# Performance work log

Hardware: AMD Instinct MI355X
Metric: run time of the kernel (lower is better)

## Reference

```python
import jax, jax.numpy as jnp
import numpy as np

IN_FEATURES = 512
NUM_KNOTS = 64
XMIN = -3.0
XMAX = 3.0


def setup_inputs() -> dict:
    key = jax.random.key(0)
    kx, kc = jax.random.split(key)
    x = jax.random.normal(kx, (65536, IN_FEATURES), dtype=jnp.float32)
    coeffs = jax.random.normal(kc, (IN_FEATURES, NUM_KNOTS), dtype=jnp.float32) * 0.01
    return {"x": x, "coeffs": coeffs}


def reference(x, coeffs):
    # x: (B, F); coeffs: (F, K). Piecewise-linear spline per feature, summed over features.
    K = coeffs.shape[1]
    t = (x - XMIN) / (XMAX - XMIN) * (K - 1)          # (B, F)
    t0 = jnp.clip(jnp.floor(t).astype(jnp.int32), 0, K - 2)
    w1 = t - t0.astype(t.dtype)
    w0 = 1.0 - w1
    feat_idx = jnp.arange(coeffs.shape[0])[None, :]    # (1, F) broadcast with (B, F) indices
    c0 = coeffs[feat_idx, t0]                          # (B, F) gather
    c1 = coeffs[feat_idx, t0 + 1]
    return jnp.sum(w0 * c0 + w1 * c1, axis=1)          # (B,)
```

## Files before the change

kernel.cpp:

```cpp
#include <hip/hip_runtime.h>


#define TILE_B 64
#define CHUNK_F 128
#define NCHUNK 4
#define LSTRIDE 129
#define FPW 32

__global__ __launch_bounds__(256, 4)
void spline_kernel(const float* __restrict__ x,
                   const float* __restrict__ coeffs,
                   float* __restrict__ out)
{
    __shared__ float ldsX[TILE_B * LSTRIDE];
    __shared__ float ldsR[4 * TILE_B];

    const int t    = threadIdx.x;
    const int lane = t & 63;
    const int w    = t >> 6;
    const long rowBase = (long)blockIdx.x * TILE_B;

    float acc0 = 0.0f, acc1 = 0.0f;

    for (int ch = 0; ch < NCHUNK; ++ch) {
        const int cbase = ch * CHUNK_F;
        __syncthreads();
        #pragma unroll
        for (int s = 0; s < 8; ++s) {
            int i4 = s * 256 + t;
            int r  = i4 >> 5;
            int c4 = i4 & 31;
            const float4 v = *reinterpret_cast<const float4*>(
                x + (rowBase + r) * 512 + cbase + c4 * 4);
            float* dst = &ldsX[r * LSTRIDE + c4 * 4];
            dst[0] = v.x; dst[1] = v.y; dst[2] = v.z; dst[3] = v.w;
        }
        __syncthreads();
        #pragma unroll 8
        for (int j = 0; j < FPW; ++j) {
            const int fc = w * FPW + j;
            const int f  = cbase + fc;
            const float cr = coeffs[f * 64 + lane];
            const float xv = ldsX[lane * LSTRIDE + fc];
            const float tt  = (xv + 3.0f) * 10.5f;
            float t0f = floorf(tt);
            t0f = fminf(fmaxf(t0f, 0.0f), 62.0f);
            const int t0 = (int)t0f;
            const float c0 = __shfl(cr, t0, 64);
            const float c1 = __shfl(cr, t0 + 1, 64);
            const float w1 = tt - t0f;
            if (j & 1) acc1 += c0 + w1 * (c1 - c0);
            else       acc0 += c0 + w1 * (c1 - c0);
        }
    }

    ldsR[w * TILE_B + lane] = acc0 + acc1;
    __syncthreads();
    if (t < TILE_B) {
        float r = ldsR[t] + ldsR[TILE_B + t] + ldsR[2 * TILE_B + t] + ldsR[3 * TILE_B + t];
        out[rowBase + t] = r;
    }
}

extern "C" void kernel_launch(void* const* d_in, const int* in_sizes, int n_in,
                              void* d_out, int out_size, void* d_ws, size_t ws_size,
                              hipStream_t stream) {
    const float* x      = (const float*)d_in[0];
    const float* coeffs = (const float*)d_in[1];
    float* out = (float*)d_out;
    (void)in_sizes; (void)n_in; (void)out_size; (void)d_ws; (void)ws_size;

    dim3 grid(65536 / TILE_B);
    dim3 block(256);
    spline_kernel<<<grid, block, 0, stream>>>(x, coeffs, out);
}
```

Baseline: 34.82 us.

## Rewrite spline kernel with packed bf16 coefficient table in LDS and lane-per-feature layout

Each block now builds a 64KB LDS table per 256-feature half. Every entry packs a bf16 base coefficient and a bf16 slope, and entries are rotated per feature to avoid bank conflicts. Each lane reads x with float4 loads straight from global memory, does one LDS lookup per feature instead of two shuffles, and reduces rows with butterfly shuffles. Blocks are 1024 threads covering 128 rows. This removes the x staging through LDS and the cross-lane shuffles, but rounding coefficients to bf16 loses precision and may break tolerance. Each block also rebuilds the coefficient table.

```diff
diff --git a/kernel.cpp b/kernel.cpp
--- a/kernel.cpp
+++ b/kernel.cpp
@@ -1,65 +1,75 @@
 #include <hip/hip_runtime.h>
+#include <stdint.h>
 
 
-#define TILE_B 64
-#define CHUNK_F 128
-#define NCHUNK 4
-#define LSTRIDE 129
-#define FPW 32
+#define ROWS_PER_BLOCK 128
 
-__global__ __launch_bounds__(256, 4)
+__device__ __forceinline__ uint32_t bf16_rne(float v) {
+    uint32_t u = __float_as_uint(v);
+    return (u + 0x7fffu + ((u >> 16) & 1u)) >> 16;
+}
+
+__global__ __launch_bounds__(1024, 4)
 void spline_kernel(const float* __restrict__ x,
                    const float* __restrict__ coeffs,
                    float* __restrict__ out)
 {
-    __shared__ float ldsX[TILE_B * LSTRIDE];
-    __shared__ float ldsR[4 * TILE_B];
+    __shared__ uint32_t T[256 * 64];
 
-    const int t    = threadIdx.x;
-    const int lane = t & 63;
-    const int w    = t >> 6;
-    const long rowBase = (long)blockIdx.x * TILE_B;
+    const int tid  = threadIdx.x;
+    const int lane = tid & 63;
+    const int w    = tid >> 6;
+    const long rowBase = (long)blockIdx.x * ROWS_PER_BLOCK;
+    const float lf   = (float)lane;
+    const float tadd = 31.5f + lf;
+    const float hi   = lf + 62.0f;
 
-    float acc0 = 0.0f, acc1 = 0.0f;
+    float accR[8] = {0.f, 0.f, 0.f, 0.f, 0.f, 0.f, 0.f, 0.f};
 
-    for (int ch = 0; ch < NCHUNK; ++ch) {
-        const int cbase = ch * CHUNK_F;
+    #pragma unroll
+    for (int c = 0; c < 2; ++c) {
         __syncthreads();
         #pragma unroll
-        for (int s = 0; s < 8; ++s) {
-            int i4 = s * 256 + t;
-            int r  = i4 >> 5;
-            int c4 = i4 & 31;
-            const float4 v = *reinterpret_cast<const float4*>(
-                x + (rowBase + r) * 512 + cbase + c4 * 4);
-            float* dst = &ldsX[r * LSTRIDE + c4 * 4];
-            dst[0] = v.x; dst[1] = v.y; dst[2] = v.z; dst[3] = v.w;
+        for (int it = 0; it < 16; ++it) {
+            const int idx = it * 1024 + tid;
+            const int fl  = idx >> 6;
+            const int k   = idx & 63;
+            const int gi  = c * 16384 + idx;
+            const float c0 = coeffs[gi];
+            const float c1 = coeffs[gi + (k < 63 ? 1 : 0)];
+            const int kp  = (k + (fl >> 2)) & 63;
+            T[(idx & ~63) | kp] = (bf16_rne(c0) << 16) | bf16_rne(c1 - c0);
         }
         __syncthreads();
-        #pragma unroll 8
-        for (int j = 0; j < FPW; ++j) {
-            const int fc = w * FPW + j;
-            const int f  = cbase + fc;
-            const float cr = coeffs[f * 64 + lane];
-            const float xv = ldsX[lane * LSTRIDE + fc];
-            const float tt  = (xv + 3.0f) * 10.5f;
-            float t0f = floorf(tt);
-            t0f = fminf(fmaxf(t0f, 0.0f), 62.0f);
-            const int t0 = (int)t0f;
-            const float c0 = __shfl(cr, t0, 64);
-            const float c1 = __shfl(cr, t0 + 1, 64);
-            const float w1 = tt - t0f;
-            if (j & 1) acc1 += c0 + w1 * (c1 - c0);
-            else       acc0 += c0 + w1 * (c1 - c0);
+
+        const float* xb = x + (rowBase + w * 8) * 512 + c * 256 + lane * 4;
+        #pragma unroll 2
+        for (int r = 0; r < 8; ++r) {
+            const float4 v = *reinterpret_cast<const float4*>(xb + r * 512);
+            float a = 0.f;
+            #pragma unroll
+            for (int q = 0; q < 4; ++q) {
+                const float xv  = (q == 0) ? v.x : (q == 1) ? v.y : (q == 2) ? v.z : v.w;
+                const float tt  = xv * 10.5f + tadd;
+                const float t0f = fminf(fmaxf(floorf(tt), lf), hi);
+                const uint32_t g = T[(lane << 8) + (q << 6) + (((int)t0f) & 63)];
+                a += __uint_as_float(g & 0xffff0000u)
+                   + (tt - t0f) * __uint_as_float(g << 16);
+            }
+            accR[r] += a;
         }
     }
 
-    ldsR[w * TILE_B + lane] = acc0 + acc1;
-    __syncthreads();
-    if (t < TILE_B) {
-        float r = ldsR[t] + ldsR[TILE_B + t] + ldsR[2 * TILE_B + t] + ldsR[3 * TILE_B + t];
-        out[rowBase + t] = r;
+    float stash = 0.f;
+    #pragma unroll
+    for (int r = 0; r < 8; ++r) {
+        float s = accR[r];
+        #pragma unroll
+        for (int m = 1; m < 64; m <<= 1)
+            s += __shfl_xor(s, m, 64);
+        if (lane == r) stash = s;
     }
+    if (lane < 8) out[rowBase + w * 8 + lane] = stash;
 }
 
 extern "C" void kernel_launch(void* const* d_in, const int* in_sizes, int n_in,
@@ -70,7 +80,7 @@
     float* out = (float*)d_out;
     (void)in_sizes; (void)n_in; (void)out_size; (void)d_ws; (void)ws_size;
 
-    dim3 grid(65536 / TILE_B);
-    dim3 block(256);
+    dim3 grid(65536 / ROWS_PER_BLOCK);
+    dim3 block(1024);
     spline_kernel<<<grid, block, 0, stream>>>(x, coeffs, out);
 }
```

After: 36.68 us. +5.3%, slower.
